# Kernel tuning notes

Measured on AMD Instinct MI355X. Metric: run time of the kernel, lower is better.

The kernel has to match this reference:

```python
import jax, jax.numpy as jnp
import numpy as np

BN_EPS = 1e-5
L2_EPS = 1e-12
TEMP = 0.01


def _fc(x, W, b, gamma, beta, mean, var, normalize):
    # Linear -> ReLU -> BatchNorm1d (eval mode, running stats) [-> L2 normalize]
    y = jnp.maximum(x @ W.T + b, 0.0)
    y = gamma * (y - mean) * jax.lax.rsqrt(var + BN_EPS) + beta
    if normalize:
        n = jnp.linalg.norm(y, axis=-1, keepdims=True)
        y = y / jnp.maximum(n, L2_EPS)
    return y


def setup_inputs() -> dict:
    key = jax.random.key(0)
    B, n, m = 8, 64, 2048
    inp_d0, con_d0, d1, d2, K = 1024, 2048, 2048, 2048, 7
    ks = jax.random.split(key, 16)
    s = 0.02
    inp = {
        'x': jax.random.normal(ks[0], (B, n, inp_d0, K, K), jnp.float32),
        'x_context': jax.random.normal(ks[1], (B, m, con_d0), jnp.float32),
        'num_valid_context_items': jax.random.randint(ks[2], (B, 1), 1, m + 1, jnp.int32),
        'q_W': jax.random.normal(ks[3], (d1, inp_d0)) * s,
        'q_b': jnp.zeros((d1,)),
        'q_gamma': jnp.ones((d1,)),
        'q_beta': jnp.zeros((d1,)),
        'q_mean': jax.random.normal(ks[4], (d1,)) * s,
        'q_var': jax.random.uniform(ks[5], (d1,), minval=0.5, maxval=1.5),
        'k_W': jax.random.normal(ks[6], (d1, con_d0)) * s,
        'k_b': jnp.zeros((d1,)),
        'k_gamma': jnp.ones((d1,)),
        'k_beta': jnp.zeros((d1,)),
        'k_mean': jax.random.normal(ks[7], (d1,)) * s,
        'k_var': jax.random.uniform(ks[8], (d1,), minval=0.5, maxval=1.5),
        'v_W': jax.random.normal(ks[9], (d2, con_d0)) * s,
        'v_b': jnp.zeros((d2,)),
        'v_gamma': jnp.ones((d2,)),
        'v_beta': jnp.zeros((d2,)),
        'v_mean': jax.random.normal(ks[10], (d2,)) * s,
        'v_var': jax.random.uniform(ks[11], (d2,), minval=0.5, maxval=1.5),
        'f_W': jax.random.normal(ks[12], (inp_d0, d2)) * s,
        'f_b': jnp.zeros((inp_d0,)),
        'f_gamma': jnp.ones((inp_d0,)),
        'f_beta': jnp.zeros((inp_d0,)),
        'f_mean': jax.random.normal(ks[13], (inp_d0,)) * s,
        'f_var': jax.random.uniform(ks[14], (inp_d0,), minval=0.5, maxval=1.5),
    }
    return inp


def reference(x, x_context, num_valid_context_items,
              q_W, q_b, q_gamma, q_beta, q_mean, q_var,
              k_W, k_b, k_gamma, k_beta, k_mean, k_var,
              v_W, v_b, v_gamma, v_beta, v_mean, v_var,
              f_W, f_b, f_gamma, f_beta, f_mean, f_var):
    # x: [B, n, D, K, K]; x_context: [B, m, C]; num_valid: [B, 1]
    A_pool = x.mean(axis=(-2, -1))                                  # [B, n, D]
    queries = _fc(A_pool, q_W, q_b, q_gamma, q_beta, q_mean, q_var, True)   # [B, n, d1]
    keys = _fc(x_context, k_W, k_b, k_gamma, k_beta, k_mean, k_var, True)   # [B, m, d1]
    values = _fc(x_context, v_W, v_b, v_gamma, v_beta, v_mean, v_var, True) # [B, m, d2]
    weights = jnp.einsum('bnd,bmd->bnm', queries, keys)             # [B, n, m]
    m = keys.shape[1]
    valid = jnp.arange(m)[None, :] < num_valid_context_items        # [B, m] bool
    weights = jnp.where(valid[:, None, :], weights, -jnp.inf)
    values = values * valid[:, :, None]
    weights = jax.nn.softmax(weights / TEMP, axis=-1)
    wv = jnp.einsum('bnm,bmd->bnd', weights, values)                # [B, n, d2]
    f_context = _fc(wv, f_W, f_b, f_gamma, f_beta, f_mean, f_var, False)    # [B, n, D]
    return x + f_context[..., None, None]
```

## Files before the change

kernel.cpp:

```cpp
#include <hip/hip_runtime.h>

typedef _Float16 f16;
typedef _Float16 f16x8 __attribute__((ext_vector_type(8)));
typedef _Float16 f16x4 __attribute__((ext_vector_type(4)));
typedef float f32x4 __attribute__((ext_vector_type(4)));
typedef float fv4 __attribute__((ext_vector_type(4)));

#define BN_EPS 1e-5f

constexpr int EPI_RAW = 0;
constexpr int EPI_HALF_NORM = 2;
constexpr int EPI_HALF = 3;
constexpr int EPI_BN_F32 = 4;
constexpr int EPI_HALF_NORM_T = 5;

__device__ __forceinline__ void gload_lds16(const void* g, void* l) {
  __builtin_amdgcn_global_load_lds(
      (const __attribute__((address_space(1))) unsigned int*)g,
      (__attribute__((address_space(3))) unsigned int*)l, 16, 0, 0);
}

#define LDSA(d0, d1, d2, d3, par, kk, mi0)            \
  {                                                   \
    const int ab_ = (par)*65536 + (kk)*16384 + aoff;  \
    d0 = ldf(ab_ + (((mi0) + 0) << 10));              \
    d1 = ldf(ab_ + (((mi0) + 1) << 10));              \
    d2 = ldf(ab_ + (((mi0) + 2) << 10));              \
    d3 = ldf(ab_ + (((mi0) + 3) << 10));              \
  }
#define LDSB(d0, d1, d2, d3, par, kk)                 \
  {                                                   \
    const int bb_ = (par)*65536 + (kk)*16384 + boff;  \
    d0 = ldf(bb_ + (0 << 10));                        \
    d1 = ldf(bb_ + (1 << 10));                        \
    d2 = ldf(bb_ + (2 << 10));                        \
    d3 = ldf(bb_ + (3 << 10));                        \
  }
#define MM16(a0, a1, a2, a3, b0, b1, b2, b3, mi0)                              \
  __builtin_amdgcn_s_setprio(1);                                               \
  acc[(mi0) + 0][0] = __builtin_amdgcn_mfma_f32_16x16x32_f16(a0, b0, acc[(mi0) + 0][0], 0, 0, 0); \
  acc[(mi0) + 0][1] = __builtin_amdgcn_mfma_f32_16x16x32_f16(a0, b1, acc[(mi0) + 0][1], 0, 0, 0); \
  acc[(mi0) + 0][2] = __builtin_amdgcn_mfma_f32_16x16x32_f16(a0, b2, acc[(mi0) + 0][2], 0, 0, 0); \
  acc[(mi0) + 0][3] = __builtin_amdgcn_mfma_f32_16x16x32_f16(a0, b3, acc[(mi0) + 0][3], 0, 0, 0); \
  acc[(mi0) + 1][0] = __builtin_amdgcn_mfma_f32_16x16x32_f16(a1, b0, acc[(mi0) + 1][0], 0, 0, 0); \
  acc[(mi0) + 1][1] = __builtin_amdgcn_mfma_f32_16x16x32_f16(a1, b1, acc[(mi0) + 1][1], 0, 0, 0); \
  acc[(mi0) + 1][2] = __builtin_amdgcn_mfma_f32_16x16x32_f16(a1, b2, acc[(mi0) + 1][2], 0, 0, 0); \
  acc[(mi0) + 1][3] = __builtin_amdgcn_mfma_f32_16x16x32_f16(a1, b3, acc[(mi0) + 1][3], 0, 0, 0); \
  acc[(mi0) + 2][0] = __builtin_amdgcn_mfma_f32_16x16x32_f16(a2, b0, acc[(mi0) + 2][0], 0, 0, 0); \
  acc[(mi0) + 2][1] = __builtin_amdgcn_mfma_f32_16x16x32_f16(a2, b1, acc[(mi0) + 2][1], 0, 0, 0); \
  acc[(mi0) + 2][2] = __builtin_amdgcn_mfma_f32_16x16x32_f16(a2, b2, acc[(mi0) + 2][2], 0, 0, 0); \
  acc[(mi0) + 2][3] = __builtin_amdgcn_mfma_f32_16x16x32_f16(a2, b3, acc[(mi0) + 2][3], 0, 0, 0); \
  acc[(mi0) + 3][0] = __builtin_amdgcn_mfma_f32_16x16x32_f16(a3, b0, acc[(mi0) + 3][0], 0, 0, 0); \
  acc[(mi0) + 3][1] = __builtin_amdgcn_mfma_f32_16x16x32_f16(a3, b1, acc[(mi0) + 3][1], 0, 0, 0); \
  acc[(mi0) + 3][2] = __builtin_amdgcn_mfma_f32_16x16x32_f16(a3, b2, acc[(mi0) + 3][2], 0, 0, 0); \
  acc[(mi0) + 3][3] = __builtin_amdgcn_mfma_f32_16x16x32_f16(a3, b3, acc[(mi0) + 3][3], 0, 0, 0); \
  __builtin_amdgcn_s_setprio(0);

template <int EPI>
__global__ __launch_bounds__(512, 1) void gemm8_kernel(
    const f16* __restrict__ A, const f16* __restrict__ Bh, int N, int K,
    int gx, f16* __restrict__ Ch, const float* __restrict__ bias,
    const float* __restrict__ gamma, const float* __restrict__ beta,
    const float* __restrict__ mean, const float* __restrict__ var,
    float* __restrict__ norm2) {
  __shared__ __align__(16) char smem[131072];

  const int nwg = gridDim.x;
  const int bid = blockIdx.x;
  const int swz = (bid & 7) * (nwg >> 3) + (bid >> 3);
  const int brow = (swz / gx) * 256;
  const int bcol = (swz % gx) * 256;

  const int tid = threadIdx.x;
  const int lane = tid & 63;
  const int w = tid >> 6;
  const int wm = w >> 2;
  const int wn = w & 3;
  const int l15 = lane & 15;
  const int l4 = lane >> 4;

  const int NT = K >> 6;

  const int c0 = tid ^ ((tid >> 3) & 3);
  const int srow = c0 >> 2;
  const int sk = (c0 & 3) * 8;
  const size_t gA0 = (size_t)(brow + srow) * K + sk;
  const size_t gB0 = (size_t)(bcol + srow) * K + sk;
  const size_t gstep = (size_t)128 * K;
  char* const ldst = smem + tid * 16;

  auto STAGE = [&](int v, int par, int op, int kk) {
    if (v >= NT) return;
    const int k0 = v * 64 + kk * 32;
    const f16* g = (op == 0) ? (A + gA0 + k0) : (Bh + gB0 + k0);
    char* l = ldst + par * 65536 + op * 32768 + kk * 16384;
    gload_lds16(g, l);
    gload_lds16(g + gstep, l + 8192);
  };

  f32x4 acc[8][4] = {};

  const int kx16 = (l4 ^ ((l15 >> 1) & 3)) * 16;
  const int aoff = ((wm * 128 + l15) << 6) + kx16;
  const int boff = 32768 + ((wn * 64 + l15) << 6) + kx16;

  auto ldf = [&](int off) -> f16x8 { return *(const f16x8*)(smem + off); };
  auto BAR = [&]() { __builtin_amdgcn_s_barrier(); };
  auto VMID = [&](int tcur) {
    if (tcur + 2 >= NT)
      asm volatile("s_waitcnt vmcnt(0)" ::: "memory");
    else
      asm volatile("s_waitcnt vmcnt(4)" ::: "memory");
  };
  auto VEND = [&](int tcur) {
    if (tcur + 2 < NT) asm volatile("s_waitcnt vmcnt(4)" ::: "memory");
  };

  f16x8 aX0, aX1, aX2, aX3, aY0, aY1, aY2, aY3;
  f16x8 bX0, bX1, bX2, bX3, bY0, bY1, bY2, bY3;

  STAGE(0, 0, 0, 0);
  STAGE(0, 0, 1, 0);
  STAGE(0, 0, 0, 1);
  STAGE(0, 0, 1, 1);
  STAGE(1, 1, 0, 0);
  STAGE(1, 1, 1, 0);
  asm volatile("s_waitcnt vmcnt(4)" ::: "memory");
  __builtin_amdgcn_s_barrier();

  LDSA(aX0, aX1, aX2, aX3, 0, 0, 0);
  LDSB(bX0, bX1, bX2, bX3, 0, 0);

  for (int t = 0; t < NT; t += 2) {
    STAGE(t + 1, 1, 0, 1);
    MM16(aX0, aX1, aX2, aX3, bX0, bX1, bX2, bX3, 0);
    LDSA(aY0, aY1, aY2, aY3, 0, 0, 4);
    BAR();
    STAGE(t + 1, 1, 1, 1);
    MM16(aY0, aY1, aY2, aY3, bX0, bX1, bX2, bX3, 4);
    LDSA(aX0, aX1, aX2, aX3, 0, 1, 0);
    LDSB(bY0, bY1, bY2, bY3, 0, 1);
    BAR();
    STAGE(t + 2, 0, 0, 0);
    MM16(aX0, aX1, aX2, aX3, bY0, bY1, bY2, bY3, 0);
    LDSA(aY0, aY1, aY2, aY3, 0, 1, 4);
    BAR();
    STAGE(t + 2, 0, 1, 0);
    VMID(t);
    MM16(aY0, aY1, aY2, aY3, bY0, bY1, bY2, bY3, 4);
    LDSA(aX0, aX1, aX2, aX3, 1, 0, 0);
    LDSB(bX0, bX1, bX2, bX3, 1, 0);
    BAR();
    STAGE(t + 2, 0, 0, 1);
    MM16(aX0, aX1, aX2, aX3, bX0, bX1, bX2, bX3, 0);
    LDSA(aY0, aY1, aY2, aY3, 1, 0, 4);
    BAR();
    STAGE(t + 2, 0, 1, 1);
    MM16(aY0, aY1, aY2, aY3, bX0, bX1, bX2, bX3, 4);
    LDSA(aX0, aX1, aX2, aX3, 1, 1, 0);
    LDSB(bY0, bY1, bY2, bY3, 1, 1);
    BAR();
    STAGE(t + 3, 1, 0, 0);
    MM16(aX0, aX1, aX2, aX3, bY0, bY1, bY2, bY3, 0);
    LDSA(aY0, aY1, aY2, aY3, 1, 1, 4);
    BAR();
    STAGE(t + 3, 1, 1, 0);
    VEND(t);
    MM16(aY0, aY1, aY2, aY3, bY0, bY1, bY2, bY3, 4);
    LDSA(aX0, aX1, aX2, aX3, 0, 0, 0);
    LDSB(bX0, bX1, bX2, bX3, 0, 0);
    BAR();
  }

  if constexpr (EPI == EPI_HALF_NORM_T) {
    float colsum[4] = {0.f, 0.f, 0.f, 0.f};
#pragma unroll
    for (int mi = 0; mi < 8; ++mi) {
#pragma unroll
      for (int jj = 0; jj < 4; ++jj) {
        const int grow = brow + wm * 128 + mi * 16 + l4 * 4 + jj;
        const float bb = bias[grow], gg = gamma[grow], mm = mean[grow];
        const float vv = var[grow], be = beta[grow];
#pragma unroll
        for (int ni = 0; ni < 4; ++ni) {
          const int gcol = bcol + wn * 64 + ni * 16 + l15;
          float y = fmaxf(acc[mi][ni][jj] + bb, 0.0f);
          y = gg * (y - mm) / sqrtf(vv + BN_EPS) + be;
          Ch[(size_t)grow * N + gcol] = (f16)y;
          colsum[ni] += y * y;
        }
      }
    }
#pragma unroll
    for (int ni = 0; ni < 4; ++ni) {
      float s = colsum[ni];
      s += __shfl_xor(s, 16);
      s += __shfl_xor(s, 32);
      if (l4 == 0)
        atomicAdd(&norm2[bcol + wn * 64 + ni * 16 + l15], s);
    }
  } else {
#pragma unroll
    for (int mi = 0; mi < 8; ++mi) {
#pragma unroll
      for (int jj = 0; jj < 4; ++jj) {
        const int grow = brow + wm * 128 + mi * 16 + l4 * 4 + jj;
        float nsum = 0.0f;
#pragma unroll
        for (int ni = 0; ni < 4; ++ni) {
          const int gcol = bcol + wn * 64 + ni * 16 + l15;
          float y = fmaxf(acc[mi][ni][jj] + bias[gcol], 0.0f);
          y = gamma[gcol] * (y - mean[gcol]) / sqrtf(var[gcol] + BN_EPS) +
              beta[gcol];
          Ch[(size_t)grow * N + gcol] = (f16)y;
          nsum += y * y;
        }
        nsum += __shfl_xor(nsum, 1);
        nsum += __shfl_xor(nsum, 2);
        nsum += __shfl_xor(nsum, 4);
        nsum += __shfl_xor(nsum, 8);
        if (l15 == 0) atomicAdd(&norm2[grow], nsum);
      }
    }
  }
}

template <int BM, int BN, int EPI>
__global__ __launch_bounds__(256, 2) void gemm_kernel(
    const f16* __restrict__ Ah, const f16* __restrict__ Bh, int M, int N,
    int K, long long sAb, long long sBb, long long sCb,
    float* __restrict__ Cf, f16* __restrict__ Ch,
    const float* __restrict__ bias, const float* __restrict__ gamma,
    const float* __restrict__ beta, const float* __restrict__ mean,
    const float* __restrict__ var, float* __restrict__ norm2) {
  (void)M;
  constexpr int BK = 32;
  constexpr int WM = BM / 2, WN = BN / 2;
  constexpr int FM = WM / 16, FN = WN / 16;

  __shared__ __align__(16) f16 lds[(BM + BN) * BK];
  f16* sA = lds;
  f16* sB = lds + BM * BK;

  const int b = blockIdx.z;
  const f16* pA = Ah + (size_t)b * sAb;
  const f16* pB = Bh + (size_t)b * sBb;

  const int brow = blockIdx.y * BM, bcol = blockIdx.x * BN;
  const int t = threadIdx.x, wave = t >> 6, lane = t & 63;
  const int wr = wave >> 1, wc = wave & 1;

  f32x4 acc[FM][FN] = {};

  constexpr int A_CH = BM / 16, B_CH = BN / 16;
  constexpr int TOT = A_CH + B_CH;

  const int srow = lane >> 2;
  const int scol = (lane & 3) * 8;
  const int lr = lane & 15;
  const int lkb = (lane >> 4) * 8;

  for (int k0 = 0; k0 < K; k0 += BK) {
    for (int id = wave; id < TOT; id += 4) {
      const f16* g;
      f16* l;
      if (id < A_CH) {
        g = pA + (size_t)(brow + id * 16 + srow) * K + k0 + scol;
        l = sA + id * 16 * BK;
      } else {
        int c = id - A_CH;
        g = pB + (size_t)(bcol + c * 16 + srow) * K + k0 + scol;
        l = sB + c * 16 * BK;
      }
      gload_lds16(g, l);
    }
    asm volatile("s_waitcnt vmcnt(0)" ::: "memory");
    __syncthreads();

    f16x8 fa[FM], fb[FN];
#pragma unroll
    for (int mi = 0; mi < FM; ++mi)
      fa[mi] = *(const f16x8*)(sA + (size_t)(wr * WM + mi * 16 + lr) * BK + lkb);
#pragma unroll
    for (int ni = 0; ni < FN; ++ni)
      fb[ni] = *(const f16x8*)(sB + (size_t)(wc * WN + ni * 16 + lr) * BK + lkb);
#pragma unroll
    for (int mi = 0; mi < FM; ++mi)
#pragma unroll
      for (int ni = 0; ni < FN; ++ni)
        acc[mi][ni] = __builtin_amdgcn_mfma_f32_16x16x32_f16(fa[mi], fb[ni],
                                                             acc[mi][ni], 0, 0, 0);
    __syncthreads();
  }

#pragma unroll
  for (int mi = 0; mi < FM; ++mi) {
#pragma unroll
    for (int j = 0; j < 4; ++j) {
      const int grow = brow + wr * WM + mi * 16 + (lane >> 4) * 4 + j;
      float nsum = 0.0f;
#pragma unroll
      for (int ni = 0; ni < FN; ++ni) {
        const int gcol = bcol + wc * WN + ni * 16 + lr;
        float val = acc[mi][ni][j];
        if constexpr (EPI == EPI_RAW) {
          Cf[(size_t)b * sCb + (size_t)grow * N + gcol] = val;
        } else if constexpr (EPI == EPI_HALF) {
          Ch[(size_t)b * sCb + (size_t)grow * N + gcol] = (f16)val;
        } else {
          float y = fmaxf(val + bias[gcol], 0.0f);
          y = gamma[gcol] * (y - mean[gcol]) / sqrtf(var[gcol] + BN_EPS) +
              beta[gcol];
          if constexpr (EPI == EPI_BN_F32) {
            Cf[(size_t)grow * N + gcol] = y;
          } else {
            Ch[(size_t)grow * N + gcol] = (f16)y;
            nsum += y * y;
          }
        }
      }
      if constexpr (EPI == EPI_HALF_NORM) {
        nsum += __shfl_xor(nsum, 1);
        nsum += __shfl_xor(nsum, 2);
        nsum += __shfl_xor(nsum, 4);
        nsum += __shfl_xor(nsum, 8);
        if (lr == 0) atomicAdd(&norm2[grow], nsum);
      }
    }
  }
}

__global__ __launch_bounds__(256) void cvt_multi_kernel(
    const float* __restrict__ s0, f16* __restrict__ d0,
    const float* __restrict__ s1, f16* __restrict__ d1,
    const float* __restrict__ s2, f16* __restrict__ d2,
    const float* __restrict__ s3, f16* __restrict__ d3,
    const float* __restrict__ s4, f16* __restrict__ d4, int c0, int c1,
    int c2, int c3, int c4) {
  int i = blockIdx.x * 256 + threadIdx.x;
  if (i >= c4) return;
  const float* s;
  f16* d;
  int j;
  if (i < c0) {
    s = s0; d = d0; j = i;
  } else if (i < c1) {
    s = s1; d = d1; j = i - c0;
  } else if (i < c2) {
    s = s2; d = d2; j = i - c1;
  } else if (i < c3) {
    s = s3; d = d3; j = i - c2;
  } else {
    s = s4; d = d4; j = i - c3;
  }
  fv4 v = ((const fv4*)s)[j];
  f16x4 h;
#pragma unroll
  for (int k = 0; k < 4; ++k) h[k] = (f16)v[k];
  ((f16x4*)d)[j] = h;
}

__global__ __launch_bounds__(256) void pool_kernel(const float* __restrict__ x,
                                                   f16* __restrict__ ah) {
  int bn = blockIdx.x;
  const float* base = x + (size_t)bn * 1024 * 49;
  for (int d = threadIdx.x; d < 1024; d += 256) {
    const float* p = base + (size_t)d * 49;
    float s = 0.f;
#pragma unroll
    for (int j = 0; j < 49; ++j) s += p[j];
    ah[(size_t)bn * 1024 + d] = (f16)(s / 49.0f);
  }
}

__global__ __launch_bounds__(256) void softmax_kernel(
    const float* __restrict__ raw, const float* __restrict__ qn2,
    const float* __restrict__ kn2, const float* __restrict__ vn2,
    const int* __restrict__ nvalid, f16* __restrict__ wgt) {
  const int n = blockIdx.x;
  const int b = blockIdx.y;
  const int row = b * 64 + n;
  const float* r = raw + (size_t)row * 2048;
  const int nv = nvalid[b];
  const float qs = 100.0f / fmaxf(sqrtf(qn2[row]), 1e-12f);

  __shared__ float sl[2048];
  __shared__ float red[4];
  const int t = threadIdx.x;

  float mx = -3.0e38f;
  for (int m = t; m < 2048; m += 256) {
    float v = -3.0e38f;
    if (m < nv) {
      float ks = 1.0f / fmaxf(sqrtf(kn2[b * 2048 + m]), 1e-12f);
      v = r[m] * qs * ks;
    }
    sl[m] = v;
    mx = fmaxf(mx, v);
  }
#pragma unroll
  for (int s = 32; s; s >>= 1) mx = fmaxf(mx, __shfl_xor(mx, s));
  if ((t & 63) == 0) red[t >> 6] = mx;
  __syncthreads();
  mx = fmaxf(fmaxf(red[0], red[1]), fmaxf(red[2], red[3]));
  __syncthreads();

  float sum = 0.f;
  for (int m = t; m < 2048; m += 256) {
    float e = (m < nv) ? __expf(sl[m] - mx) : 0.0f;
    sl[m] = e;
    sum += e;
  }
#pragma unroll
  for (int s = 32; s; s >>= 1) sum += __shfl_xor(sum, s);
  if ((t & 63) == 0) red[t >> 6] = sum;
  __syncthreads();
  sum = red[0] + red[1] + red[2] + red[3];
  const float inv = 1.0f / sum;

  for (int m = t; m < 2048; m += 256) {
    float vs = 1.0f / fmaxf(sqrtf(vn2[b * 2048 + m]), 1e-12f);
    wgt[(size_t)row * 2048 + m] = (f16)(sl[m] * inv * vs);
  }
}

__global__ __launch_bounds__(256) void add_kernel(const float* __restrict__ x,
                                                  const float* __restrict__ fc,
                                                  float* __restrict__ out,
                                                  int n4) {
  int i = blockIdx.x * 256 + threadIdx.x;
  if (i >= n4) return;
  fv4 v = ((const fv4*)x)[i];
  int e = i * 4;
#pragma unroll
  for (int j = 0; j < 4; ++j) v[j] += fc[(e + j) / 49];
  ((fv4*)out)[i] = v;
}

extern "C" void kernel_launch(void* const* d_in, const int* in_sizes, int n_in,
                              void* d_out, int out_size, void* d_ws,
                              size_t ws_size, hipStream_t stream) {
  (void)in_sizes; (void)n_in; (void)out_size; (void)ws_size;
  const float* x = (const float*)d_in[0];
  const float* xc = (const float*)d_in[1];
  const int* nvp = (const int*)d_in[2];
  const float* qW = (const float*)d_in[3];
  const float* qB = (const float*)d_in[4];
  const float* qG = (const float*)d_in[5];
  const float* qBe = (const float*)d_in[6];
  const float* qM = (const float*)d_in[7];
  const float* qV = (const float*)d_in[8];
  const float* kW = (const float*)d_in[9];
  const float* kB = (const float*)d_in[10];
  const float* kG = (const float*)d_in[11];
  const float* kBe = (const float*)d_in[12];
  const float* kM = (const float*)d_in[13];
  const float* kV = (const float*)d_in[14];
  const float* vW = (const float*)d_in[15];
  const float* vB = (const float*)d_in[16];
  const float* vG = (const float*)d_in[17];
  const float* vBe = (const float*)d_in[18];
  const float* vM = (const float*)d_in[19];
  const float* vV = (const float*)d_in[20];
  const float* fW = (const float*)d_in[21];
  const float* fB = (const float*)d_in[22];
  const float* fG = (const float*)d_in[23];
  const float* fBe = (const float*)d_in[24];
  const float* fM = (const float*)d_in[25];
  const float* fV = (const float*)d_in[26];
  float* out = (float*)d_out;

  const int NRq = 512;
  const int NRc = 16384;
  const int Dd = 1024, Cc = 2048, D1 = 2048, D2 = 2048, Mm = 2048;

  char* p = (char*)d_ws;
  auto take = [&](size_t bytes) -> char* {
    char* r = p;
    p += (bytes + 255) & ~(size_t)255;
    return r;
  };
  f16* xch = (f16*)take((size_t)NRc * Cc * 2);
  f16* kh = (f16*)take((size_t)NRc * D1 * 2);
  f16* vT = (f16*)take((size_t)NRc * D2 * 2);
  f16* qWh = (f16*)take((size_t)D1 * Dd * 2);
  f16* kWh = (f16*)take((size_t)D1 * Cc * 2);
  f16* vWh = (f16*)take((size_t)D2 * Cc * 2);
  f16* fWh = (f16*)take((size_t)Dd * D2 * 2);
  f16* Aph = (f16*)take((size_t)NRq * Dd * 2);
  f16* qh = (f16*)take((size_t)NRq * D1 * 2);
  float* norms = (float*)take((size_t)(NRq + 2 * NRc) * 4);
  float* qn2 = norms;
  float* kn2 = norms + NRq;
  float* vn2 = norms + NRq + NRc;
  float* raw = (float*)take((size_t)NRq * Mm * 4);
  f16* wgt = (f16*)take((size_t)NRq * Mm * 2);
  f16* wvh = (f16*)take((size_t)NRq * D2 * 2);
  float* fctx = (float*)take((size_t)NRq * Dd * 4);

  const int n4_0 = NRc * Cc / 4;
  const int n4_1 = D1 * Dd / 4;
  const int n4_2 = D1 * Cc / 4;
  const int n4_3 = D2 * Cc / 4;
  const int n4_4 = Dd * D2 / 4;
  const int cum0 = n4_0, cum1 = cum0 + n4_1, cum2 = cum1 + n4_2,
            cum3 = cum2 + n4_3, cum4 = cum3 + n4_4;
  cvt_multi_kernel<<<dim3((cum4 + 255) / 256), 256, 0, stream>>>(
      xc, xch, qW, qWh, kW, kWh, vW, vWh, fW, fWh, cum0, cum1, cum2, cum3,
      cum4);
  pool_kernel<<<dim3(512), 256, 0, stream>>>(x, Aph);
  hipMemsetAsync(norms, 0, (size_t)(NRq + 2 * NRc) * 4, stream);

  gemm_kernel<32, 128, EPI_HALF_NORM>
      <<<dim3(D1 / 128, NRq / 32, 1), 256, 0, stream>>>(
          Aph, qWh, NRq, D1, Dd, 0, 0, 0, nullptr, qh, qB, qG, qBe, qM, qV,
          qn2);
  gemm8_kernel<EPI_HALF_NORM>
      <<<dim3((NRc / 256) * (D1 / 256)), 512, 0, stream>>>(
          xch, kWh, D1, Cc, D1 / 256, kh, kB, kG, kBe, kM, kV, kn2);
  gemm8_kernel<EPI_HALF_NORM_T>
      <<<dim3((D2 / 256) * (NRc / 256)), 512, 0, stream>>>(
          vWh, xch, NRc, Cc, NRc / 256, vT, vB, vG, vBe, vM, vV, vn2);
  gemm_kernel<32, 128, EPI_RAW><<<dim3(Mm / 128, 2, 8), 256, 0, stream>>>(
      qh, kh, 64, Mm, D1, (long long)64 * D1, (long long)Mm * D1,
      (long long)64 * Mm, raw, nullptr, nullptr, nullptr, nullptr, nullptr,
      nullptr, nullptr);
  softmax_kernel<<<dim3(64, 8), 256, 0, stream>>>(raw, qn2, kn2, vn2, nvp, wgt);
  gemm_kernel<32, 128, EPI_HALF><<<dim3(D2 / 128, 2, 8), 256, 0, stream>>>(
      wgt, vT, 64, D2, Mm, (long long)64 * Mm, (long long)D2 * Mm,
      (long long)64 * D2, nullptr, wvh, nullptr, nullptr, nullptr, nullptr,
      nullptr, nullptr);
  gemm_kernel<32, 128, EPI_BN_F32>
      <<<dim3(Dd / 128, NRq / 32, 1), 256, 0, stream>>>(
          wvh, fWh, NRq, Dd, D2, 0, 0, 0, fctx, nullptr, fB, fG, fBe, fM, fV,
          nullptr);
  add_kernel<<<dim3(25690112 / 4 / 256), 256, 0, stream>>>(x, fctx, out,
                                                           25690112 / 4);
}
```

Baseline: 584.6 us.

## Switch big GEMM kernel from 16x16x32 to 32x32x16 MFMA tiles

Replaces the 16x16x32 f16 MFMA inner loop of the 256x256 GEMM with 32x32x16 MFMA instructions that accumulate into f32x16 registers. The LDS fragment read offsets and the epilogue's row/column mapping are rewritten to match the 32x32 output layout. The aim is to cut LDS reads per FLOP and instruction-issue overhead. The risks are LDS bank conflicts from the dropped XOR swizzle and possibly wrong K-slice indexing if the new offsets do not match how the staged tiles are stored.

```diff
diff --git a/kernel.cpp b/kernel.cpp
--- a/kernel.cpp
+++ b/kernel.cpp
@@ -4,6 +4,7 @@
 typedef _Float16 f16x8 __attribute__((ext_vector_type(8)));
 typedef _Float16 f16x4 __attribute__((ext_vector_type(4)));
 typedef float f32x4 __attribute__((ext_vector_type(4)));
+typedef float f32x16 __attribute__((ext_vector_type(16)));
 typedef float fv4 __attribute__((ext_vector_type(4)));
 
 #define BN_EPS 1e-5f
@@ -20,40 +21,32 @@
       (__attribute__((address_space(3))) unsigned int*)l, 16, 0, 0);
 }
 
-#define LDSA(d0, d1, d2, d3, par, kk, mi0)            \
-  {                                                   \
-    const int ab_ = (par)*65536 + (kk)*16384 + aoff;  \
-    d0 = ldf(ab_ + (((mi0) + 0) << 10));              \
-    d1 = ldf(ab_ + (((mi0) + 1) << 10));              \
-    d2 = ldf(ab_ + (((mi0) + 2) << 10));              \
-    d3 = ldf(ab_ + (((mi0) + 3) << 10));              \
-  }
-#define LDSB(d0, d1, d2, d3, par, kk)                 \
-  {                                                   \
-    const int bb_ = (par)*65536 + (kk)*16384 + boff;  \
-    d0 = ldf(bb_ + (0 << 10));                        \
-    d1 = ldf(bb_ + (1 << 10));                        \
-    d2 = ldf(bb_ + (2 << 10));                        \
-    d3 = ldf(bb_ + (3 << 10));                        \
-  }
-#define MM16(a0, a1, a2, a3, b0, b1, b2, b3, mi0)                              \
-  __builtin_amdgcn_s_setprio(1);                                               \
-  acc[(mi0) + 0][0] = __builtin_amdgcn_mfma_f32_16x16x32_f16(a0, b0, acc[(mi0) + 0][0], 0, 0, 0); \
-  acc[(mi0) + 0][1] = __builtin_amdgcn_mfma_f32_16x16x32_f16(a0, b1, acc[(mi0) + 0][1], 0, 0, 0); \
-  acc[(mi0) + 0][2] = __builtin_amdgcn_mfma_f32_16x16x32_f16(a0, b2, acc[(mi0) + 0][2], 0, 0, 0); \
-  acc[(mi0) + 0][3] = __builtin_amdgcn_mfma_f32_16x16x32_f16(a0, b3, acc[(mi0) + 0][3], 0, 0, 0); \
-  acc[(mi0) + 1][0] = __builtin_amdgcn_mfma_f32_16x16x32_f16(a1, b0, acc[(mi0) + 1][0], 0, 0, 0); \
-  acc[(mi0) + 1][1] = __builtin_amdgcn_mfma_f32_16x16x32_f16(a1, b1, acc[(mi0) + 1][1], 0, 0, 0); \
-  acc[(mi0) + 1][2] = __builtin_amdgcn_mfma_f32_16x16x32_f16(a1, b2, acc[(mi0) + 1][2], 0, 0, 0); \
-  acc[(mi0) + 1][3] = __builtin_amdgcn_mfma_f32_16x16x32_f16(a1, b3, acc[(mi0) + 1][3], 0, 0, 0); \
-  acc[(mi0) + 2][0] = __builtin_amdgcn_mfma_f32_16x16x32_f16(a2, b0, acc[(mi0) + 2][0], 0, 0, 0); \
-  acc[(mi0) + 2][1] = __builtin_amdgcn_mfma_f32_16x16x32_f16(a2, b1, acc[(mi0) + 2][1], 0, 0, 0); \
-  acc[(mi0) + 2][2] = __builtin_amdgcn_mfma_f32_16x16x32_f16(a2, b2, acc[(mi0) + 2][2], 0, 0, 0); \
-  acc[(mi0) + 2][3] = __builtin_amdgcn_mfma_f32_16x16x32_f16(a2, b3, acc[(mi0) + 2][3], 0, 0, 0); \
-  acc[(mi0) + 3][0] = __builtin_amdgcn_mfma_f32_16x16x32_f16(a3, b0, acc[(mi0) + 3][0], 0, 0, 0); \
-  acc[(mi0) + 3][1] = __builtin_amdgcn_mfma_f32_16x16x32_f16(a3, b1, acc[(mi0) + 3][1], 0, 0, 0); \
-  acc[(mi0) + 3][2] = __builtin_amdgcn_mfma_f32_16x16x32_f16(a3, b2, acc[(mi0) + 3][2], 0, 0, 0); \
-  acc[(mi0) + 3][3] = __builtin_amdgcn_mfma_f32_16x16x32_f16(a3, b3, acc[(mi0) + 3][3], 0, 0, 0); \
+#define LDSA(d0, d1, d2, d3, par, kk, bp)                      \
+  {                                                            \
+    const int ab_ = (par)*65536 + (kk)*16384 + aoff + (bp)*1024; \
+    d0 = ldf(ab_);                          \
+    d1 = ldf(ab_ + 8192);                   \
+    d2 = ldf(ab_ + 512);                    \
+    d3 = ldf(ab_ + 8192 + 512);             \
+  }
+#define LDSB(d0, d1, d2, d3, par, kk)                          \
+  {                                                            \
+    const int bb_ = (par)*65536 + (kk)*16384 + boff;           \
+    d0 = ldf(bb_);                                 \
+    d1 = ldf(bb_ + 8192);                          \
+    d2 = ldf(bb_ + 512);                           \
+    d3 = ldf(bb_ + 8192 + 512);                    \
+  }
+#define MM8(a0, a1, a2, a3, b0, b1, b2, b3, bp)                                        \
+  __builtin_amdgcn_s_setprio(1);                                                       \
+  acc[2*(bp)+0][0] = __builtin_amdgcn_mfma_f32_32x32x16_f16(a0, b0, acc[2*(bp)+0][0], 0, 0, 0); \
+  acc[2*(bp)+0][0] = __builtin_amdgcn_mfma_f32_32x32x16_f16(a1, b1, acc[2*(bp)+0][0], 0, 0, 0); \
+  acc[2*(bp)+0][1] = __builtin_amdgcn_mfma_f32_32x32x16_f16(a0, b2, acc[2*(bp)+0][1], 0, 0, 0); \
+  acc[2*(bp)+0][1] = __builtin_amdgcn_mfma_f32_32x32x16_f16(a1, b3, acc[2*(bp)+0][1], 0, 0, 0); \
+  acc[2*(bp)+1][0] = __builtin_amdgcn_mfma_f32_32x32x16_f16(a2, b0, acc[2*(bp)+1][0], 0, 0, 0); \
+  acc[2*(bp)+1][0] = __builtin_amdgcn_mfma_f32_32x32x16_f16(a3, b1, acc[2*(bp)+1][0], 0, 0, 0); \
+  acc[2*(bp)+1][1] = __builtin_amdgcn_mfma_f32_32x32x16_f16(a2, b2, acc[2*(bp)+1][1], 0, 0, 0); \
+  acc[2*(bp)+1][1] = __builtin_amdgcn_mfma_f32_32x32x16_f16(a3, b3, acc[2*(bp)+1][1], 0, 0, 0); \
   __builtin_amdgcn_s_setprio(0);
 
 template <int EPI>
@@ -76,8 +69,8 @@
   const int w = tid >> 6;
   const int wm = w >> 2;
   const int wn = w & 3;
-  const int l15 = lane & 15;
-  const int l4 = lane >> 4;
+  const int l31 = lane & 31;
+  const int ls = lane >> 5;
 
   const int NT = K >> 6;
 
@@ -98,11 +91,10 @@
     gload_lds16(g + gstep, l + 8192);
   };
 
-  f32x4 acc[8][4] = {};
-
-  const int kx16 = (l4 ^ ((l15 >> 1) & 3)) * 16;
-  const int aoff = ((wm * 128 + l15) << 6) + kx16;
-  const int boff = 32768 + ((wn * 64 + l15) << 6) + kx16;
+  f32x16 acc[4][2] = {};
+
+  const int aoff = ls * 4096 + ((wm * 128 + l31) << 4);
+  const int boff = 32768 + ls * 4096 + ((wn * 64 + l31) << 4);
 
   auto ldf = [&](int off) -> f16x8 { return *(const f16x8*)(smem + off); };
   auto BAR = [&]() { __builtin_amdgcn_s_barrier(); };
@@ -133,83 +125,84 @@
 
   for (int t = 0; t < NT; t += 2) {
     STAGE(t + 1, 1, 0, 1);
-    MM16(aX0, aX1, aX2, aX3, bX0, bX1, bX2, bX3, 0);
-    LDSA(aY0, aY1, aY2, aY3, 0, 0, 4);
+    MM8(aX0, aX1, aX2, aX3, bX0, bX1, bX2, bX3, 0);
+    LDSA(aY0, aY1, aY2, aY3, 0, 0, 1);
     BAR();
     STAGE(t + 1, 1, 1, 1);
-    MM16(aY0, aY1, aY2, aY3, bX0, bX1, bX2, bX3, 4);
+    MM8(aY0, aY1, aY2, aY3, bX0, bX1, bX2, bX3, 1);
     LDSA(aX0, aX1, aX2, aX3, 0, 1, 0);
     LDSB(bY0, bY1, bY2, bY3, 0, 1);
     BAR();
     STAGE(t + 2, 0, 0, 0);
-    MM16(aX0, aX1, aX2, aX3, bY0, bY1, bY2, bY3, 0);
-    LDSA(aY0, aY1, aY2, aY3, 0, 1, 4);
+    MM8(aX0, aX1, aX2, aX3, bY0, bY1, bY2, bY3, 0);
+    LDSA(aY0, aY1, aY2, aY3, 0, 1, 1);
     BAR();
     STAGE(t + 2, 0, 1, 0);
     VMID(t);
-    MM16(aY0, aY1, aY2, aY3, bY0, bY1, bY2, bY3, 4);
+    MM8(aY0, aY1, aY2, aY3, bY0, bY1, bY2, bY3, 1);
     LDSA(aX0, aX1, aX2, aX3, 1, 0, 0);
     LDSB(bX0, bX1, bX2, bX3, 1, 0);
     BAR();
     STAGE(t + 2, 0, 0, 1);
-    MM16(aX0, aX1, aX2, aX3, bX0, bX1, bX2, bX3, 0);
-    LDSA(aY0, aY1, aY2, aY3, 1, 0, 4);
+    MM8(aX0, aX1, aX2, aX3, bX0, bX1, bX2, bX3, 0);
+    LDSA(aY0, aY1, aY2, aY3, 1, 0, 1);
     BAR();
     STAGE(t + 2, 0, 1, 1);
-    MM16(aY0, aY1, aY2, aY3, bX0, bX1, bX2, bX3, 4);
+    MM8(aY0, aY1, aY2, aY3, bX0, bX1, bX2, bX3, 1);
     LDSA(aX0, aX1, aX2, aX3, 1, 1, 0);
     LDSB(bY0, bY1, bY2, bY3, 1, 1);
     BAR();
     STAGE(t + 3, 1, 0, 0);
-    MM16(aX0, aX1, aX2, aX3, bY0, bY1, bY2, bY3, 0);
-    LDSA(aY0, aY1, aY2, aY3, 1, 1, 4);
+    MM8(aX0, aX1, aX2, aX3, bY0, bY1, bY2, bY3, 0);
+    LDSA(aY0, aY1, aY2, aY3, 1, 1, 1);
     BAR();
     STAGE(t + 3, 1, 1, 0);
     VEND(t);
-    MM16(aY0, aY1, aY2, aY3, bY0, bY1, bY2, bY3, 4);
+    MM8(aY0, aY1, aY2, aY3, bY0, bY1, bY2, bY3, 1);
     LDSA(aX0, aX1, aX2, aX3, 0, 0, 0);
     LDSB(bX0, bX1, bX2, bX3, 0, 0);
     BAR();
   }
 
   if constexpr (EPI == EPI_HALF_NORM_T) {
-    float colsum[4] = {0.f, 0.f, 0.f, 0.f};
-#pragma unroll
-    for (int mi = 0; mi < 8; ++mi) {
-#pragma unroll
-      for (int jj = 0; jj < 4; ++jj) {
-        const int grow = brow + wm * 128 + mi * 16 + l4 * 4 + jj;
+    float colsum[2] = {0.f, 0.f};
+#pragma unroll
+    for (int blk = 0; blk < 4; ++blk) {
+#pragma unroll
+      for (int reg = 0; reg < 16; ++reg) {
+        const int grow =
+            brow + wm * 128 + blk * 32 + (reg & 3) + 8 * (reg >> 2) + 4 * ls;
         const float bb = bias[grow], gg = gamma[grow], mm = mean[grow];
         const float vv = var[grow], be = beta[grow];
 #pragma unroll
-        for (int ni = 0; ni < 4; ++ni) {
-          const int gcol = bcol + wn * 64 + ni * 16 + l15;
-          float y = fmaxf(acc[mi][ni][jj] + bb, 0.0f);
+        for (int cb = 0; cb < 2; ++cb) {
+          const int gcol = bcol + wn * 64 + cb * 32 + l31;
+          float y = fmaxf(acc[blk][cb][reg] + bb, 0.0f);
           y = gg * (y - mm) / sqrtf(vv + BN_EPS) + be;
           Ch[(size_t)grow * N + gcol] = (f16)y;
-          colsum[ni] += y * y;
+          colsum[cb] += y * y;
         }
       }
     }
 #pragma unroll
-    for (int ni = 0; ni < 4; ++ni) {
-      float s = colsum[ni];
-      s += __shfl_xor(s, 16);
+    for (int cb = 0; cb < 2; ++cb) {
+      float s = colsum[cb];
       s += __shfl_xor(s, 32);
-      if (l4 == 0)
-        atomicAdd(&norm2[bcol + wn * 64 + ni * 16 + l15], s);
+      if (ls == 0)
+        atomicAdd(&norm2[bcol + wn * 64 + cb * 32 + l31], s);
     }
   } else {
 #pragma unroll
-    for (int mi = 0; mi < 8; ++mi) {
-#pragma unroll
-      for (int jj = 0; jj < 4; ++jj) {
-        const int grow = brow + wm * 128 + mi * 16 + l4 * 4 + jj;
+    for (int blk = 0; blk < 4; ++blk) {
+#pragma unroll
+      for (int reg = 0; reg < 16; ++reg) {
+        const int grow =
+            brow + wm * 128 + blk * 32 + (reg & 3) + 8 * (reg >> 2) + 4 * ls;
         float nsum = 0.0f;
 #pragma unroll
-        for (int ni = 0; ni < 4; ++ni) {
-          const int gcol = bcol + wn * 64 + ni * 16 + l15;
-          float y = fmaxf(acc[mi][ni][jj] + bias[gcol], 0.0f);
+        for (int cb = 0; cb < 2; ++cb) {
+          const int gcol = bcol + wn * 64 + cb * 32 + l31;
+          float y = fmaxf(acc[blk][cb][reg] + bias[gcol], 0.0f);
           y = gamma[gcol] * (y - mean[gcol]) / sqrtf(var[gcol] + BN_EPS) +
               beta[gcol];
           Ch[(size_t)grow * N + gcol] = (f16)y;
@@ -219,7 +212,8 @@
         nsum += __shfl_xor(nsum, 2);
         nsum += __shfl_xor(nsum, 4);
         nsum += __shfl_xor(nsum, 8);
-        if (l15 == 0) atomicAdd(&norm2[grow], nsum);
+        nsum += __shfl_xor(nsum, 16);
+        if (l31 == 0) atomicAdd(&norm2[grow], nsum);
       }
     }
   }
```

Result: slower. 633.5 us (+8.4%).
